# Kernel tuning notes

Hardware: AMD Instinct MI355X
Metric: run time of the kernel (lower is better)

## Reference

```python
import jax, jax.numpy as jnp
import numpy as np
from jax import lax

# --- config (matches init_kwargs) ---
H = 1024          # hidden_size
I = 704           # moe_intermediate_size (per expert)
E = 32            # n_routed_experts
G = 8             # n_group
TOPK_GROUP = 3    # topk_group
K = 6             # num_experts_per_tok
N_SHARED = 2      # n_shared_experts -> shared intermediate = N_SHARED * I
SCALE = 1.0       # routed_scaling_factor
T = 2048          # number of tokens
CAP = 2 * (T * K) // E


def setup_inputs() -> dict:
    key = jax.random.key(0)
    ks = jax.random.split(key, 8)
    s = 0.02  # initializer_range
    Is = N_SHARED * I
    return {
        "x": jax.random.normal(ks[0], (T, H), jnp.float32),
        "gate_w": s * jax.random.normal(ks[1], (E, H), jnp.float32),   # router
        "w_gate": s * jax.random.normal(ks[2], (E, H, I), jnp.float32),
        "w_up":   s * jax.random.normal(ks[3], (E, H, I), jnp.float32),
        "w_down": s * jax.random.normal(ks[4], (E, I, H), jnp.float32),
        "sw_gate": s * jax.random.normal(ks[5], (H, Is), jnp.float32),
        "sw_up":   s * jax.random.normal(ks[6], (H, Is), jnp.float32),
        "sw_down": s * jax.random.normal(ks[7], (Is, H), jnp.float32),
    }


def _moe_forward(x, gate_w, w_gate, w_up, w_down, sw_gate, sw_up, sw_down):
    # ---- router: softmax scores + group-limited top-k (topk_method='gready') ----
    logits = x @ gate_w.T                                  # [T, E]
    scores = jax.nn.softmax(logits, axis=-1)               # [T, E]
    group_scores = scores.reshape(T, G, E // G).max(-1)    # [T, G]
    _, gidx = lax.top_k(group_scores, TOPK_GROUP)          # [T, topk_group]
    gmask = jnp.zeros((T, G), scores.dtype).at[jnp.arange(T)[:, None], gidx].set(1.0)
    emask = jnp.repeat(gmask, E // G, axis=1)              # [T, E]
    masked_scores = jnp.where(emask > 0, scores, 0.0)
    topk_w, topk_idx = lax.top_k(masked_scores, K)         # [T, K]
    # norm_topk_prob=False -> weights are raw softmax scores * routed_scaling_factor
    topk_w = topk_w * SCALE

    # ---- dispatch: sort assignments by expert, scatter into [E, CAP, H] buffers ----
    flat_e = topk_idx.reshape(-1)                          # [T*K]
    order = jnp.argsort(flat_e)
    se = flat_e[order]                                     # sorted expert ids
    tok = order // K                                       # source token of each slot
    counts = jax.ops.segment_sum(jnp.ones_like(flat_e), flat_e, num_segments=E)
    starts = jnp.cumsum(counts) - counts
    pos = jnp.arange(T * K) - starts[se]                   # position within expert
    valid = pos < CAP
    pos_w = jnp.where(valid, pos, CAP)                     # overflow slot CAP (sliced off)
    xbuf = jnp.zeros((E, CAP + 1, H), x.dtype).at[se, pos_w].set(x[tok])
    xb = xbuf[:, :CAP]                                     # [E, CAP, H]

    # ---- grouped expert MLPs: silu(x Wg) * (x Wu) @ Wd ----
    g = jnp.einsum("ech,ehi->eci", xb, w_gate)
    u = jnp.einsum("ech,ehi->eci", xb, w_up)
    yb = jnp.einsum("eci,eih->ech", jax.nn.silu(g) * u, w_down)  # [E, CAP, H]

    # ---- combine: gather back and weighted-scatter to tokens ----
    y_flat = yb[se, jnp.minimum(pos, CAP - 1)] * valid[:, None].astype(x.dtype)
    wts = topk_w.reshape(-1)[order]                        # [T*K]
    routed = jnp.zeros((T, H), x.dtype).at[tok].add(y_flat * wts[:, None])

    # ---- shared experts MLP (intermediate = n_shared * moe_inter) ----
    sg = jax.nn.silu(x @ sw_gate) * (x @ sw_up)
    shared = sg @ sw_down

    return routed + shared                                 # [T, H]


def reference(x, gate_w, w_gate, w_up, w_down, sw_gate, sw_up, sw_down):
    return _moe_forward(x, gate_w, w_gate, w_up, w_down, sw_gate, sw_up, sw_down)
```

## Files before the change

### kernel.cpp

```cpp
#include <hip/hip_runtime.h>
#include <hip/hip_bf16.h>

#define H 1024
#define I_DIM 704
#define E 32
#define TOPK_GROUP 3
#define K_TOP 6
#define T_TOK 2048
#define CAP 768
#define IS_DIM 1408
#define NCHUNK 192

typedef __attribute__((ext_vector_type(8))) short short8v;
typedef __attribute__((ext_vector_type(4))) float f32x4;

__device__ __forceinline__ unsigned short f2bfbits(float f) {
  unsigned u = __float_as_uint(f);
  unsigned r = (u + 0x7fffu + ((u >> 16) & 1u)) >> 16;
  return (unsigned short)r;
}
__device__ __forceinline__ unsigned packbf2(float lo, float hi) {
  __hip_bfloat162 h = __float22bfloat162_rn(make_float2(lo, hi));
  unsigned u; __builtin_memcpy(&u, &h, 4); return u;
}
__device__ __forceinline__ float bf2f(unsigned short b) {
  return __uint_as_float(((unsigned)b) << 16);
}
__device__ __forceinline__ void gload_lds16(const short* g, short* l) {
  __builtin_amdgcn_global_load_lds(
      (const __attribute__((address_space(1))) unsigned int*)g,
      (__attribute__((address_space(3))) unsigned int*)l, 16, 0, 0);
}

__global__ void cast_x_kernel(const float* __restrict__ x, short* __restrict__ xb) {
  size_t i = ((size_t)blockIdx.x * 256 + threadIdx.x) * 4;
  float4 v = *(const float4*)(x + i);
  short4 s;
  s.x = (short)f2bfbits(v.x); s.y = (short)f2bfbits(v.y);
  s.z = (short)f2bfbits(v.z); s.w = (short)f2bfbits(v.w);
  *(short4*)(xb + i) = s;
}

__global__ __launch_bounds__(64) void gating_kernel(const float* __restrict__ x,
                                                    const float* __restrict__ gw,
                                                    int* __restrict__ tidx,
                                                    float* __restrict__ tw) {
  int t = blockIdx.x;
  int lane = threadIdx.x;
  int e = lane & 31, half = lane >> 5;
  const float4* xr4 = (const float4*)(x + (size_t)t * H + half * 512);
  const float4* wr4 = (const float4*)(gw + (size_t)e * H + half * 512);
  double acc = 0.0;
  #pragma unroll 4
  for (int j = 0; j < 128; ++j) {
    float4 a = xr4[j], b = wr4[j];
    acc += (double)a.x * b.x + (double)a.y * b.y + (double)a.z * b.z + (double)a.w * b.w;
  }
  acc += __shfl_down(acc, 32);
  double lg = acc;
  double m = lg;
  #pragma unroll
  for (int off = 16; off >= 1; off >>= 1) {
    double o = __shfl_xor(m, off);
    if (o > m) m = o;
  }
  double p = exp(lg - m);
  double sum = p;
  #pragma unroll
  for (int off = 16; off >= 1; off >>= 1) sum += __shfl_xor(sum, off);
  p /= sum;
  double gmax = p;
  { double o = __shfl_xor(gmax, 1); if (o > gmax) gmax = o;
    o = __shfl_xor(gmax, 2); if (o > gmax) gmax = o; }
  bool gsel = false;
  double gv = gmax;
  #pragma unroll
  for (int it = 0; it < TOPK_GROUP; ++it) {
    double v = gv; int gi = e >> 2;
    #pragma unroll
    for (int off = 16; off >= 1; off >>= 1) {
      double ov = __shfl_xor(v, off);
      int oi = __shfl_xor(gi, off);
      if (ov > v || (ov == v && oi < gi)) { v = ov; gi = oi; }
    }
    if ((e >> 2) == gi) { gsel = true; gv = -1e300; }
  }
  double mp = gsel ? p : 0.0;
  #pragma unroll
  for (int it = 0; it < K_TOP; ++it) {
    double v = mp; int ei = e;
    #pragma unroll
    for (int off = 16; off >= 1; off >>= 1) {
      double ov = __shfl_xor(v, off);
      int oi = __shfl_xor(ei, off);
      if (ov > v || (ov == v && oi < ei)) { v = ov; ei = oi; }
    }
    if (lane == 0) { tidx[t * K_TOP + it] = ei; tw[t * K_TOP + it] = (float)v; }
    if (e == ei) mp = -2.0;
  }
}

__global__ __launch_bounds__(64) void hist_kernel(const int* __restrict__ tidx,
                                                  int* __restrict__ chunk_hist) {
  __shared__ int h[E];
  int c = blockIdx.x, lane = threadIdx.x;
  if (lane < E) h[lane] = 0;
  __syncthreads();
  int te = tidx[c * 64 + lane];
  atomicAdd(&h[te], 1);
  __syncthreads();
  if (lane < E) chunk_hist[c * E + lane] = h[lane];
}

__global__ __launch_bounds__(1024) void scan_kernel(const int* __restrict__ chunk_hist,
                                                    int* __restrict__ chunk_base,
                                                    int* __restrict__ cnt) {
  __shared__ int h[NCHUNK * E];
  int t = threadIdx.x;
  for (int i = t; i < NCHUNK * E; i += 1024) h[i] = chunk_hist[i];
  __syncthreads();
  if (t < E) {
    int run = 0;
    for (int c = 0; c < NCHUNK; ++c) {
      int v = h[c * E + t];
      h[c * E + t] = run;
      run += v;
    }
    cnt[t] = run < CAP ? run : CAP;
  }
  __syncthreads();
  for (int i = t; i < NCHUNK * E; i += 1024) chunk_base[i] = h[i];
}

__global__ __launch_bounds__(64) void place_kernel(const int* __restrict__ tidx,
                                                   const int* __restrict__ chunk_base,
                                                   int* __restrict__ token_list,
                                                   int* __restrict__ sid) {
  int c = blockIdx.x, lane = threadIdx.x;
  int idx = c * 64 + lane;
  int te = tidx[idx];
  unsigned long long mymask = 0;
  #pragma unroll
  for (int e = 0; e < E; ++e) {
    unsigned long long bal = __ballot(te == e);
    if (te == e) mymask = bal;
  }
  int rank = __popcll(mymask & ((1ull << lane) - 1ull));
  int pos = chunk_base[c * E + te] + rank;
  int s = -1;
  if (pos < CAP) {
    token_list[te * CAP + pos] = idx / K_TOP;
    s = te * CAP + pos;
  }
  sid[idx] = s;
}

__global__ __launch_bounds__(256) void gateup_kernel(
    const short* __restrict__ Xb, const float* __restrict__ Wg, const float* __restrict__ Wu,
    short* __restrict__ Sout, const int* __restrict__ tlist, const int* __restrict__ cnt_dev,
    int Nld, long long wstride, long long sstride) {
  int e = blockIdx.z;
  int cnt = cnt_dev ? cnt_dev[e] : T_TOK;
  int row0 = blockIdx.y * 128;
  if (row0 >= cnt) return;
  int col0 = blockIdx.x * 64;
  const float* wg = Wg + (long long)e * wstride;
  const float* wu = Wu + (long long)e * wstride;
  short* sbase = Sout + (long long)e * sstride;

  __shared__ __align__(16) short As[128 * 32];
  __shared__ __align__(16) short Bgs[64 * 32];
  __shared__ __align__(16) short Bus[64 * 32];

  int tid = threadIdx.x;
  int lane = tid & 63, wave = tid >> 6;

  int rr = tid >> 2, ch = tid & 3;
  int ra0 = row0 + rr, ra1 = ra0 + 64;
  if (tlist) {
    const int* tl = tlist + e * CAP;
    ra0 = tl[min(ra0, cnt - 1)];
    ra1 = tl[min(ra1, cnt - 1)];
  }
  const short* pa0 = Xb + (size_t)ra0 * H + ch * 8;
  const short* pa1 = Xb + (size_t)ra1 * H + ch * 8;
  short* ldsA0 = &As[(wave * 16) * 32];
  short* ldsA1 = &As[(64 + wave * 16) * 32];

  int bn = lane, kb = wave * 8;
  const float* pg = wg + (size_t)kb * Nld + col0 + bn;
  const float* pu = wu + (size_t)kb * Nld + col0 + bn;
  short* ldsBg = &Bgs[bn * 32 + kb];
  short* ldsBu = &Bus[bn * 32 + kb];

  int wm = wave & 1, wn = wave >> 1;
  int c = lane & 15, q = lane >> 4;
  const short* fA = &As[(wm * 64 + c) * 32 + q * 8];
  const short* fBg = &Bgs[(wn * 32 + c) * 32 + q * 8];
  const short* fBu = &Bus[(wn * 32 + c) * 32 + q * 8];

  f32x4 accg[4][2], accu[4][2];
  #pragma unroll
  for (int i = 0; i < 4; ++i)
    #pragma unroll
    for (int j = 0; j < 2; ++j) {
      accg[i][j] = (f32x4){0.f, 0.f, 0.f, 0.f};
      accu[i][j] = (f32x4){0.f, 0.f, 0.f, 0.f};
    }

  for (int k0 = 0; k0 < H; k0 += 32) {
    float gv[8], uv[8];
    const float* pgk = pg + (size_t)k0 * Nld;
    const float* puk = pu + (size_t)k0 * Nld;
    #pragma unroll
    for (int j = 0; j < 8; ++j) {
      gv[j] = pgk[(size_t)j * Nld];
      uv[j] = puk[(size_t)j * Nld];
    }
    __syncthreads();
    gload_lds16(pa0 + k0, ldsA0);
    gload_lds16(pa1 + k0, ldsA1);
    uint4 wvg, wvu;
    wvg.x = packbf2(gv[0], gv[1]); wvg.y = packbf2(gv[2], gv[3]);
    wvg.z = packbf2(gv[4], gv[5]); wvg.w = packbf2(gv[6], gv[7]);
    wvu.x = packbf2(uv[0], uv[1]); wvu.y = packbf2(uv[2], uv[3]);
    wvu.z = packbf2(uv[4], uv[5]); wvu.w = packbf2(uv[6], uv[7]);
    *(uint4*)ldsBg = wvg;
    *(uint4*)ldsBu = wvu;
    __syncthreads();
    short8v a[4], bg[2], bu[2];
    #pragma unroll
    for (int mi = 0; mi < 4; ++mi) a[mi] = *(const short8v*)(fA + mi * 16 * 32);
    #pragma unroll
    for (int ni = 0; ni < 2; ++ni) {
      bg[ni] = *(const short8v*)(fBg + ni * 16 * 32);
      bu[ni] = *(const short8v*)(fBu + ni * 16 * 32);
    }
    #pragma unroll
    for (int mi = 0; mi < 4; ++mi)
      #pragma unroll
      for (int ni = 0; ni < 2; ++ni) {
        accg[mi][ni] = __builtin_amdgcn_mfma_f32_16x16x32_bf16(a[mi], bg[ni], accg[mi][ni], 0, 0, 0);
        accu[mi][ni] = __builtin_amdgcn_mfma_f32_16x16x32_bf16(a[mi], bu[ni], accu[mi][ni], 0, 0, 0);
      }
  }
  #pragma unroll
  for (int mi = 0; mi < 4; ++mi) {
    int rbase = row0 + wm * 64 + mi * 16 + q * 4;
    #pragma unroll
    for (int ni = 0; ni < 2; ++ni) {
      int col = col0 + wn * 32 + ni * 16 + c;
      #pragma unroll
      for (int r = 0; r < 4; ++r) {
        float g = accg[mi][ni][r], u = accu[mi][ni][r];
        float s = (g / (1.f + __expf(-g))) * u;
        sbase[(size_t)(rbase + r) * Nld + col] = (short)f2bfbits(s);
      }
    }
  }
}

__global__ __launch_bounds__(256) void down_kernel(
    const short* __restrict__ Sin, const float* __restrict__ Wd,
    float* __restrict__ outF, short* __restrict__ outY,
    const int* __restrict__ cnt_dev, int Kdim, long long wstride, long long sstride) {
  int e = blockIdx.z;
  int cnt = cnt_dev ? cnt_dev[e] : T_TOK;
  int row0 = blockIdx.y * 128;
  if (row0 >= cnt) return;
  int col0 = blockIdx.x * 128;
  const short* sb = Sin + (long long)e * sstride;
  const float* wd = Wd + (long long)e * wstride;

  __shared__ __align__(16) short As[128 * 32];
  __shared__ __align__(16) short Bs[128 * 32];

  int tid = threadIdx.x;
  int lane = tid & 63, wave = tid >> 6;
  int rr = tid >> 2, ch = tid & 3;

  const short* pa0 = sb + (size_t)(row0 + rr) * Kdim + ch * 8;
  const short* pa1 = pa0 + (size_t)64 * Kdim;
  short* ldsA0 = &As[(wave * 16) * 32];
  short* ldsA1 = &As[(64 + wave * 16) * 32];

  int bn = tid & 127, kb = (tid >> 7) * 16;
  const float* pb = wd + (size_t)kb * H + col0 + bn;
  short* ldsB = &Bs[bn * 32 + kb];

  int wm = wave & 1, wn = wave >> 1;
  int c = lane & 15, q = lane >> 4;
  const short* fA = &As[(wm * 64 + c) * 32 + q * 8];
  const short* fB = &Bs[(wn * 64 + c) * 32 + q * 8];

  f32x4 acc[4][4];
  #pragma unroll
  for (int i = 0; i < 4; ++i)
    #pragma unroll
    for (int j = 0; j < 4; ++j) acc[i][j] = (f32x4){0.f, 0.f, 0.f, 0.f};

  for (int k0 = 0; k0 < Kdim; k0 += 32) {
    float bv[16];
    const float* pbk = pb + (size_t)k0 * H;
    #pragma unroll
    for (int j = 0; j < 16; ++j) bv[j] = pbk[(size_t)j * H];
    __syncthreads();
    gload_lds16(pa0 + k0, ldsA0);
    gload_lds16(pa1 + k0, ldsA1);
    uint4 w0, w1;
    w0.x = packbf2(bv[0], bv[1]);  w0.y = packbf2(bv[2], bv[3]);
    w0.z = packbf2(bv[4], bv[5]);  w0.w = packbf2(bv[6], bv[7]);
    w1.x = packbf2(bv[8], bv[9]);  w1.y = packbf2(bv[10], bv[11]);
    w1.z = packbf2(bv[12], bv[13]); w1.w = packbf2(bv[14], bv[15]);
    *(uint4*)ldsB = w0;
    *(uint4*)(ldsB + 8) = w1;
    __syncthreads();
    short8v a[4], b[4];
    #pragma unroll
    for (int mi = 0; mi < 4; ++mi) a[mi] = *(const short8v*)(fA + mi * 16 * 32);
    #pragma unroll
    for (int ni = 0; ni < 4; ++ni) b[ni] = *(const short8v*)(fB + ni * 16 * 32);
    #pragma unroll
    for (int mi = 0; mi < 4; ++mi)
      #pragma unroll
      for (int ni = 0; ni < 4; ++ni)
        acc[mi][ni] = __builtin_amdgcn_mfma_f32_16x16x32_bf16(a[mi], b[ni], acc[mi][ni], 0, 0, 0);
  }

  if (outY) {
    #pragma unroll
    for (int mi = 0; mi < 4; ++mi) {
      int rb = row0 + wm * 64 + mi * 16 + q * 4;
      #pragma unroll
      for (int r = 0; r < 4; ++r) {
        short* yrow = outY + (size_t)(e * CAP + rb + r) * H;
        #pragma unroll
        for (int ni = 0; ni < 4; ++ni) {
          int col = col0 + wn * 64 + ni * 16 + c;
          yrow[col] = (short)f2bfbits(acc[mi][ni][r]);
        }
      }
    }
  } else {
    #pragma unroll
    for (int mi = 0; mi < 4; ++mi) {
      int rb = row0 + wm * 64 + mi * 16 + q * 4;
      #pragma unroll
      for (int ni = 0; ni < 4; ++ni) {
        int col = col0 + wn * 64 + ni * 16 + c;
        #pragma unroll
        for (int r = 0; r < 4; ++r)
          outF[(size_t)(rb + r) * H + col] = acc[mi][ni][r];
      }
    }
  }
}

__global__ __launch_bounds__(256) void combine_kernel(
    const short* __restrict__ Yr, const int* __restrict__ sid,
    const float* __restrict__ twt, float* __restrict__ out) {
  int t = blockIdx.x;
  int col = threadIdx.x * 4;
  float* op = out + (size_t)t * H + col;
  float4 o = *(float4*)op;
  #pragma unroll
  for (int k = 0; k < K_TOP; ++k) {
    int s = sid[t * K_TOP + k];
    if (s >= 0) {
      float w = twt[t * K_TOP + k];
      ushort4 y = *(const ushort4*)(Yr + (size_t)s * H + col);
      o.x += w * bf2f(y.x);
      o.y += w * bf2f(y.y);
      o.z += w * bf2f(y.z);
      o.w += w * bf2f(y.w);
    }
  }
  *(float4*)op = o;
}

extern "C" void kernel_launch(void* const* d_in, const int* in_sizes, int n_in,
                              void* d_out, int out_size, void* d_ws, size_t ws_size,
                              hipStream_t stream) {
  const float* x       = (const float*)d_in[0];
  const float* gate_w  = (const float*)d_in[1];
  const float* w_gate  = (const float*)d_in[2];
  const float* w_up    = (const float*)d_in[3];
  const float* w_down  = (const float*)d_in[4];
  const float* sw_gate = (const float*)d_in[5];
  const float* sw_up   = (const float*)d_in[6];
  const float* sw_down = (const float*)d_in[7];
  float* out = (float*)d_out;
  char* ws = (char*)d_ws;

  size_t o = 0;
  short* xb   = (short*)(ws + o); o += (size_t)T_TOK * H * 2;
  short* Sr   = (short*)(ws + o); o += (size_t)E * CAP * I_DIM * 2;
  short* Ss   = (short*)(ws + o); o += (size_t)T_TOK * IS_DIM * 2;
  short* Yr   = (short*)(ws + o); o += (size_t)E * CAP * H * 2;
  int*   tidx = (int*)(ws + o);   o += (size_t)T_TOK * K_TOP * 4;
  float* twt  = (float*)(ws + o); o += (size_t)T_TOK * K_TOP * 4;
  int*   sid  = (int*)(ws + o);   o += (size_t)T_TOK * K_TOP * 4;
  int*   tl   = (int*)(ws + o);   o += (size_t)E * CAP * 4;
  int*   cnt  = (int*)(ws + o);   o += 256;
  int*   chist = (int*)(ws + o);  o += (size_t)NCHUNK * E * 4;
  int*   cbase = (int*)(ws + o);  o += (size_t)NCHUNK * E * 4;

  cast_x_kernel<<<(T_TOK * H) / 1024, 256, 0, stream>>>(x, xb);
  gating_kernel<<<T_TOK, 64, 0, stream>>>(x, gate_w, tidx, twt);
  hist_kernel<<<NCHUNK, 64, 0, stream>>>(tidx, chist);
  scan_kernel<<<1, 1024, 0, stream>>>(chist, cbase, cnt);
  place_kernel<<<NCHUNK, 64, 0, stream>>>(tidx, cbase, tl, sid);

  gateup_kernel<<<dim3(I_DIM / 64, CAP / 128, E), 256, 0, stream>>>(
      xb, w_gate, w_up, Sr, tl, cnt, I_DIM, (long long)H * I_DIM, (long long)CAP * I_DIM);
  gateup_kernel<<<dim3(IS_DIM / 64, T_TOK / 128, 1), 256, 0, stream>>>(
      xb, sw_gate, sw_up, Ss, nullptr, nullptr, IS_DIM, 0, 0);
  down_kernel<<<dim3(H / 128, T_TOK / 128, 1), 256, 0, stream>>>(
      Ss, sw_down, out, nullptr, nullptr, IS_DIM, 0, 0);
  down_kernel<<<dim3(H / 128, CAP / 128, E), 256, 0, stream>>>(
      Sr, w_down, nullptr, Yr, cnt, I_DIM, (long long)I_DIM * H, (long long)CAP * I_DIM);
  combine_kernel<<<T_TOK, 256, 0, stream>>>(Yr, sid, twt, out);
}
```

Measured before the change: 551.1 us.

## Double-buffer A tiles and prefetch weights with XOR-swizzled LDS in expert GEMMs

Both the gate/up and down GEMM kernels now double-buffer the activation tile in LDS. While the current k-step computes, they issue the global loads for the next k-step: activations go straight to LDS and fp32 weights go into registers. Synchronisation is handled by hand with explicit s_barrier and s_waitcnt in place of paired __syncthreads. An XOR swizzle on the 16-byte chunk index is also applied to the A and B LDS layouts to reduce bank conflicts on the MFMA fragment reads. The trade-off is more LDS and registers, which may lower occupancy, and the hand-tuned vmcnt counts are fragile.

```diff
diff --git a/kernel.cpp b/kernel.cpp
--- a/kernel.cpp
+++ b/kernel.cpp
@@ -168,7 +168,7 @@
   const float* wu = Wu + (long long)e * wstride;
   short* sbase = Sout + (long long)e * sstride;
 
-  __shared__ __align__(16) short As[128 * 32];
+  __shared__ __align__(16) short As[2][128 * 32];
   __shared__ __align__(16) short Bgs[64 * 32];
   __shared__ __align__(16) short Bus[64 * 32];
 
@@ -176,28 +176,34 @@
   int lane = tid & 63, wave = tid >> 6;
 
   int rr = tid >> 2, ch = tid & 3;
+  int che = ch ^ ((rr >> 1) & 3);
   int ra0 = row0 + rr, ra1 = ra0 + 64;
   if (tlist) {
     const int* tl = tlist + e * CAP;
     ra0 = tl[min(ra0, cnt - 1)];
     ra1 = tl[min(ra1, cnt - 1)];
   }
-  const short* pa0 = Xb + (size_t)ra0 * H + ch * 8;
-  const short* pa1 = Xb + (size_t)ra1 * H + ch * 8;
-  short* ldsA0 = &As[(wave * 16) * 32];
-  short* ldsA1 = &As[(64 + wave * 16) * 32];
-
-  int bn = lane, kb = wave * 8;
-  const float* pg = wg + (size_t)kb * Nld + col0 + bn;
-  const float* pu = wu + (size_t)kb * Nld + col0 + bn;
-  short* ldsBg = &Bgs[bn * 32 + kb];
-  short* ldsBu = &Bus[bn * 32 + kb];
+  const short* pa0 = Xb + (size_t)ra0 * H + che * 8;
+  const short* pa1 = Xb + (size_t)ra1 * H + che * 8;
+  short* ldsA00 = &As[0][(wave * 16) * 32];
+  short* ldsA10 = &As[0][(64 + wave * 16) * 32];
+  short* ldsA01 = &As[1][(wave * 16) * 32];
+  short* ldsA11 = &As[1][(64 + wave * 16) * 32];
+
+  int bn = lane;
+  const float* pg = wg + (size_t)(wave * 8) * Nld + col0 + bn;
+  const float* pu = wu + (size_t)(wave * 8) * Nld + col0 + bn;
+  int kswz = (wave ^ ((bn >> 1) & 3)) * 8;
+  short* ldsBg = &Bgs[bn * 32 + kswz];
+  short* ldsBu = &Bus[bn * 32 + kswz];
 
   int wm = wave & 1, wn = wave >> 1;
   int c = lane & 15, q = lane >> 4;
-  const short* fA = &As[(wm * 64 + c) * 32 + q * 8];
-  const short* fBg = &Bgs[(wn * 32 + c) * 32 + q * 8];
-  const short* fBu = &Bus[(wn * 32 + c) * 32 + q * 8];
+  int qa = q ^ ((c >> 1) & 3);
+  const short* fA0 = &As[0][(wm * 64 + c) * 32 + qa * 8];
+  const short* fA1 = &As[1][(wm * 64 + c) * 32 + qa * 8];
+  const short* fBg = &Bgs[(wn * 32 + c) * 32 + qa * 8];
+  const short* fBu = &Bus[(wn * 32 + c) * 32 + qa * 8];
 
   f32x4 accg[4][2], accu[4][2];
   #pragma unroll
@@ -208,42 +214,64 @@
       accu[i][j] = (f32x4){0.f, 0.f, 0.f, 0.f};
     }
 
-  for (int k0 = 0; k0 < H; k0 += 32) {
-    float gv[8], uv[8];
-    const float* pgk = pg + (size_t)k0 * Nld;
-    const float* puk = pu + (size_t)k0 * Nld;
-    #pragma unroll
-    for (int j = 0; j < 8; ++j) {
-      gv[j] = pgk[(size_t)j * Nld];
-      uv[j] = puk[(size_t)j * Nld];
-    }
-    __syncthreads();
-    gload_lds16(pa0 + k0, ldsA0);
-    gload_lds16(pa1 + k0, ldsA1);
-    uint4 wvg, wvu;
-    wvg.x = packbf2(gv[0], gv[1]); wvg.y = packbf2(gv[2], gv[3]);
-    wvg.z = packbf2(gv[4], gv[5]); wvg.w = packbf2(gv[6], gv[7]);
-    wvu.x = packbf2(uv[0], uv[1]); wvu.y = packbf2(uv[2], uv[3]);
-    wvu.z = packbf2(uv[4], uv[5]); wvu.w = packbf2(uv[6], uv[7]);
-    *(uint4*)ldsBg = wvg;
-    *(uint4*)ldsBu = wvu;
-    __syncthreads();
-    short8v a[4], bg[2], bu[2];
-    #pragma unroll
-    for (int mi = 0; mi < 4; ++mi) a[mi] = *(const short8v*)(fA + mi * 16 * 32);
-    #pragma unroll
-    for (int ni = 0; ni < 2; ++ni) {
-      bg[ni] = *(const short8v*)(fBg + ni * 16 * 32);
-      bu[ni] = *(const short8v*)(fBu + ni * 16 * 32);
-    }
-    #pragma unroll
-    for (int mi = 0; mi < 4; ++mi)
-      #pragma unroll
-      for (int ni = 0; ni < 2; ++ni) {
-        accg[mi][ni] = __builtin_amdgcn_mfma_f32_16x16x32_bf16(a[mi], bg[ni], accg[mi][ni], 0, 0, 0);
-        accu[mi][ni] = __builtin_amdgcn_mfma_f32_16x16x32_bf16(a[mi], bu[ni], accu[mi][ni], 0, 0, 0);
-      }
-  }
+  float gvA[8], uvA[8], gvB[8], uvB[8];
+  gload_lds16(pa0, ldsA00);
+  gload_lds16(pa1, ldsA10);
+  #pragma unroll
+  for (int j = 0; j < 8; ++j) {
+    gvA[j] = pg[(size_t)j * Nld];
+    uvA[j] = pu[(size_t)j * Nld];
+  }
+
+#define GU_PHASE(KC, FAC, LA0, LA1, GC, UC, GN, UN, PREF)                           \
+  {                                                                                 \
+    __builtin_amdgcn_s_barrier();                                                   \
+    asm volatile("" ::: "memory");                                                  \
+    if (PREF) {                                                                     \
+      gload_lds16(pa0 + (KC) + 32, LA0);                                            \
+      gload_lds16(pa1 + (KC) + 32, LA1);                                            \
+      const float* pgk = pg + (size_t)((KC) + 32) * Nld;                            \
+      const float* puk = pu + (size_t)((KC) + 32) * Nld;                            \
+      _Pragma("unroll")                                                             \
+      for (int j = 0; j < 8; ++j) {                                                 \
+        GN[j] = pgk[(size_t)j * Nld];                                               \
+        UN[j] = puk[(size_t)j * Nld];                                               \
+      }                                                                             \
+    }                                                                               \
+    uint4 wvg, wvu;                                                                 \
+    wvg.x = packbf2(GC[0], GC[1]); wvg.y = packbf2(GC[2], GC[3]);                   \
+    wvg.z = packbf2(GC[4], GC[5]); wvg.w = packbf2(GC[6], GC[7]);                   \
+    wvu.x = packbf2(UC[0], UC[1]); wvu.y = packbf2(UC[2], UC[3]);                   \
+    wvu.z = packbf2(UC[4], UC[5]); wvu.w = packbf2(UC[6], UC[7]);                   \
+    *(uint4*)ldsBg = wvg;                                                           \
+    *(uint4*)ldsBu = wvu;                                                           \
+    asm volatile("s_waitcnt lgkmcnt(0)" ::: "memory");                              \
+    asm volatile("s_waitcnt vmcnt(18)" ::: "memory");                               \
+    __builtin_amdgcn_s_barrier();                                                   \
+    __builtin_amdgcn_sched_barrier(0);                                              \
+    short8v a[4], bg[2], bu[2];                                                     \
+    _Pragma("unroll")                                                               \
+    for (int mi = 0; mi < 4; ++mi) a[mi] = *(const short8v*)((FAC) + mi * 16 * 32); \
+    _Pragma("unroll")                                                               \
+    for (int ni = 0; ni < 2; ++ni) {                                                \
+      bg[ni] = *(const short8v*)(fBg + ni * 16 * 32);                               \
+      bu[ni] = *(const short8v*)(fBu + ni * 16 * 32);                               \
+    }                                                                               \
+    _Pragma("unroll")                                                               \
+    for (int mi = 0; mi < 4; ++mi)                                                  \
+      _Pragma("unroll")                                                             \
+      for (int ni = 0; ni < 2; ++ni) {                                              \
+        accg[mi][ni] = __builtin_amdgcn_mfma_f32_16x16x32_bf16(a[mi], bg[ni], accg[mi][ni], 0, 0, 0); \
+        accu[mi][ni] = __builtin_amdgcn_mfma_f32_16x16x32_bf16(a[mi], bu[ni], accu[mi][ni], 0, 0, 0); \
+      }                                                                             \
+  }
+
+  for (int k0 = 0; k0 < H; k0 += 64) {
+    GU_PHASE(k0,      fA0, ldsA01, ldsA11, gvA, uvA, gvB, uvB, true);
+    GU_PHASE(k0 + 32, fA1, ldsA00, ldsA10, gvB, uvB, gvA, uvA, (k0 + 64 < H));
+  }
+#undef GU_PHASE
+
   #pragma unroll
   for (int mi = 0; mi < 4; ++mi) {
     int rbase = row0 + wm * 64 + mi * 16 + q * 4;
@@ -272,26 +300,33 @@
   const short* sb = Sin + (long long)e * sstride;
   const float* wd = Wd + (long long)e * wstride;
 
-  __shared__ __align__(16) short As[128 * 32];
+  __shared__ __align__(16) short As[2][128 * 32];
   __shared__ __align__(16) short Bs[128 * 32];
 
   int tid = threadIdx.x;
   int lane = tid & 63, wave = tid >> 6;
   int rr = tid >> 2, ch = tid & 3;
-
-  const short* pa0 = sb + (size_t)(row0 + rr) * Kdim + ch * 8;
+  int che = ch ^ ((rr >> 1) & 3);
+
+  const short* pa0 = sb + (size_t)(row0 + rr) * Kdim + che * 8;
   const short* pa1 = pa0 + (size_t)64 * Kdim;
-  short* ldsA0 = &As[(wave * 16) * 32];
-  short* ldsA1 = &As[(64 + wave * 16) * 32];
-
-  int bn = tid & 127, kb = (tid >> 7) * 16;
-  const float* pb = wd + (size_t)kb * H + col0 + bn;
-  short* ldsB = &Bs[bn * 32 + kb];
+  short* ldsA00 = &As[0][(wave * 16) * 32];
+  short* ldsA10 = &As[0][(64 + wave * 16) * 32];
+  short* ldsA01 = &As[1][(wave * 16) * 32];
+  short* ldsA11 = &As[1][(64 + wave * 16) * 32];
+
+  int bn = tid & 127, w2 = tid >> 7;
+  const float* pb = wd + (size_t)(w2 * 16) * H + col0 + bn;
+  int bs = (bn >> 1) & 3;
+  short* ldsB0 = &Bs[bn * 32 + ((w2 * 2) ^ bs) * 8];
+  short* ldsB1 = &Bs[bn * 32 + ((w2 * 2 + 1) ^ bs) * 8];
 
   int wm = wave & 1, wn = wave >> 1;
   int c = lane & 15, q = lane >> 4;
-  const short* fA = &As[(wm * 64 + c) * 32 + q * 8];
-  const short* fB = &Bs[(wn * 64 + c) * 32 + q * 8];
+  int qa = q ^ ((c >> 1) & 3);
+  const short* fA0 = &As[0][(wm * 64 + c) * 32 + qa * 8];
+  const short* fA1 = &As[1][(wm * 64 + c) * 32 + qa * 8];
+  const short* fB  = &Bs[(wn * 64 + c) * 32 + qa * 8];
 
   f32x4 acc[4][4];
   #pragma unroll
@@ -299,33 +334,51 @@
     #pragma unroll
     for (int j = 0; j < 4; ++j) acc[i][j] = (f32x4){0.f, 0.f, 0.f, 0.f};
 
-  for (int k0 = 0; k0 < Kdim; k0 += 32) {
-    float bv[16];
-    const float* pbk = pb + (size_t)k0 * H;
-    #pragma unroll
-    for (int j = 0; j < 16; ++j) bv[j] = pbk[(size_t)j * H];
-    __syncthreads();
-    gload_lds16(pa0 + k0, ldsA0);
-    gload_lds16(pa1 + k0, ldsA1);
-    uint4 w0, w1;
-    w0.x = packbf2(bv[0], bv[1]);  w0.y = packbf2(bv[2], bv[3]);
-    w0.z = packbf2(bv[4], bv[5]);  w0.w = packbf2(bv[6], bv[7]);
-    w1.x = packbf2(bv[8], bv[9]);  w1.y = packbf2(bv[10], bv[11]);
-    w1.z = packbf2(bv[12], bv[13]); w1.w = packbf2(bv[14], bv[15]);
-    *(uint4*)ldsB = w0;
-    *(uint4*)(ldsB + 8) = w1;
-    __syncthreads();
-    short8v a[4], b[4];
-    #pragma unroll
-    for (int mi = 0; mi < 4; ++mi) a[mi] = *(const short8v*)(fA + mi * 16 * 32);
-    #pragma unroll
-    for (int ni = 0; ni < 4; ++ni) b[ni] = *(const short8v*)(fB + ni * 16 * 32);
-    #pragma unroll
-    for (int mi = 0; mi < 4; ++mi)
-      #pragma unroll
-      for (int ni = 0; ni < 4; ++ni)
-        acc[mi][ni] = __builtin_amdgcn_mfma_f32_16x16x32_bf16(a[mi], b[ni], acc[mi][ni], 0, 0, 0);
-  }
+  float bvA[16], bvB[16];
+  gload_lds16(pa0, ldsA00);
+  gload_lds16(pa1, ldsA10);
+  #pragma unroll
+  for (int j = 0; j < 16; ++j) bvA[j] = pb[(size_t)j * H];
+
+#define DN_PHASE(KC, FAC, LA0, LA1, BC, BND, PREF)                                  \
+  {                                                                                 \
+    __builtin_amdgcn_s_barrier();                                                   \
+    asm volatile("" ::: "memory");                                                  \
+    if (PREF) {                                                                     \
+      gload_lds16(pa0 + (KC) + 32, LA0);                                            \
+      gload_lds16(pa1 + (KC) + 32, LA1);                                            \
+      const float* pbk = pb + (size_t)((KC) + 32) * H;                              \
+      _Pragma("unroll")                                                             \
+      for (int j = 0; j < 16; ++j) BND[j] = pbk[(size_t)j * H];                     \
+    }                                                                               \
+    uint4 w0, w1;                                                                   \
+    w0.x = packbf2(BC[0], BC[1]);   w0.y = packbf2(BC[2], BC[3]);                   \
+    w0.z = packbf2(BC[4], BC[5]);   w0.w = packbf2(BC[6], BC[7]);                   \
+    w1.x = packbf2(BC[8], BC[9]);   w1.y = packbf2(BC[10], BC[11]);                 \
+    w1.z = packbf2(BC[12], BC[13]); w1.w = packbf2(BC[14], BC[15]);                 \
+    *(uint4*)ldsB0 = w0;                                                            \
+    *(uint4*)ldsB1 = w1;                                                            \
+    asm volatile("s_waitcnt lgkmcnt(0)" ::: "memory");                              \
+    asm volatile("s_waitcnt vmcnt(18)" ::: "memory");                               \
+    __builtin_amdgcn_s_barrier();                                                   \
+    __builtin_amdgcn_sched_barrier(0);                                              \
+    short8v a[4], b[4];                                                             \
+    _Pragma("unroll")                                                               \
+    for (int mi = 0; mi < 4; ++mi) a[mi] = *(const short8v*)((FAC) + mi * 16 * 32); \
+    _Pragma("unroll")                                                               \
+    for (int ni = 0; ni < 4; ++ni) b[ni] = *(const short8v*)(fB + ni * 16 * 32);    \
+    _Pragma("unroll")                                                               \
+    for (int mi = 0; mi < 4; ++mi)                                                  \
+      _Pragma("unroll")                                                             \
+      for (int ni = 0; ni < 4; ++ni)                                                \
+        acc[mi][ni] = __builtin_amdgcn_mfma_f32_16x16x32_bf16(a[mi], b[ni], acc[mi][ni], 0, 0, 0); \
+  }
+
+  for (int k0 = 0; k0 < Kdim; k0 += 64) {
+    DN_PHASE(k0,      fA0, ldsA01, ldsA11, bvA, bvB, true);
+    DN_PHASE(k0 + 32, fA1, ldsA00, ldsA10, bvB, bvA, (k0 + 64 < Kdim));
+  }
+#undef DN_PHASE
 
   if (outY) {
     #pragma unroll
```

New measurement: 548.0 us. No clear change (-0.6%).
